# Performance work log

Hardware: AMD Instinct MI355X
Metric: run time of the kernel (lower is better)

The kernel has to match this reference:

```python
import jax, jax.numpy as jnp
import numpy as np

VOCAB, D_MODEL, HEADS, PAD_ID = 32000, 512, 8, 0
D_K = D_MODEL // HEADS
EPS = 1e-5


def pos_encoding(T, d):
    pos = jnp.arange(T, dtype=jnp.float32)[:, None]              # [T,1]
    freqs = 1.0 / (10000.0 ** (jnp.arange(0, d, 2, dtype=jnp.float32) / d))
    ang = pos * freqs                                            # [T,d/2]
    pe = jnp.zeros((T, d), dtype=jnp.float32)
    pe = pe.at[:, 0::2].set(jnp.sin(ang)).at[:, 1::2].set(jnp.cos(ang))
    return pe


def layer_norm(x, g, b):
    mu = jnp.mean(x, axis=-1, keepdims=True)
    var = jnp.var(x, axis=-1, keepdims=True)
    return (x - mu) * jax.lax.rsqrt(var + EPS) * g + b


def setup_inputs() -> dict:
    key = jax.random.key(0)
    ks = jax.random.split(key, 12)
    B, T = 4, 2048
    s = 0.02
    inp = {
        "tokens": jax.random.randint(ks[0], (B, T), 0, VOCAB),
        "emb": jax.random.normal(ks[1], (VOCAB, D_MODEL), jnp.float32) * s,
        "wq": jax.random.normal(ks[2], (D_MODEL, D_MODEL), jnp.float32) * s,
        "bq": jnp.zeros((D_MODEL,), jnp.float32),
        "wk": jax.random.normal(ks[3], (D_MODEL, D_MODEL), jnp.float32) * s,
        "bk": jnp.zeros((D_MODEL,), jnp.float32),
        "wv": jax.random.normal(ks[4], (D_MODEL, D_MODEL), jnp.float32) * s,
        "bv": jnp.zeros((D_MODEL,), jnp.float32),
        "wo": jax.random.normal(ks[5], (D_MODEL, D_MODEL), jnp.float32) * s,
        "bo": jnp.zeros((D_MODEL,), jnp.float32),
        "w1": jax.random.normal(ks[6], (D_MODEL, 2 * D_MODEL), jnp.float32) * s,
        "b1": jnp.zeros((2 * D_MODEL,), jnp.float32),
        "w2": jax.random.normal(ks[7], (2 * D_MODEL, D_MODEL), jnp.float32) * s,
        "b2": jnp.zeros((D_MODEL,), jnp.float32),
        "ln1_g": jnp.ones((D_MODEL,), jnp.float32),
        "ln1_b": jnp.zeros((D_MODEL,), jnp.float32),
        "ln2_g": jnp.ones((D_MODEL,), jnp.float32),
        "ln2_b": jnp.zeros((D_MODEL,), jnp.float32),
    }
    return inp


def reference(tokens, emb, wq, bq, wk, bk, wv, bv, wo, bo,
              w1, b1, w2, b2, ln1_g, ln1_b, ln2_g, ln2_b):
    B, T = tokens.shape
    x = emb[tokens] * jnp.sqrt(jnp.float32(D_MODEL))             # [B,T,D]
    x = x + pos_encoding(T, D_MODEL)[None]                       # add PE
    q = (x @ wq + bq).reshape(B, T, HEADS, D_K)
    k = (x @ wk + bk).reshape(B, T, HEADS, D_K)
    v = (x @ wv + bv).reshape(B, T, HEADS, D_K)
    scores = jnp.einsum("bqhd,bkhd->bhqk", q, k) / jnp.sqrt(jnp.float32(D_K))
    key_pad_mask = tokens == PAD_ID                              # [B,T]
    neg = jnp.finfo(scores.dtype).min
    scores = jnp.where(key_pad_mask[:, None, None, :], neg, scores)
    attn = jax.nn.softmax(scores, axis=-1)                       # [B,H,T,T]
    av = jnp.einsum("bhqk,bkhd->bqhd", attn, v).reshape(B, T, D_MODEL)
    av = av @ wo + bo
    h = layer_norm(av + x, ln1_g, ln1_b)
    ff = jax.nn.relu(h @ w1 + b1) @ w2 + b2
    out = layer_norm(h + ff, ln2_g, ln2_b)
    return out, key_pad_mask
```

## Files before the change

### kernel.cpp

```cpp
#include <hip/hip_runtime.h>
#include <hip/hip_bf16.h>
#include <math.h>

#define D_MODEL 512
#define HEADS   8
#define D_K     64
#define T_SEQ   2048
#define B_SZ    4
#define NROWS   (B_SZ * T_SEQ)
#define KVB     64

#define BM 128
#define BN 128
#define BKG 64

typedef __attribute__((ext_vector_type(8))) short short8;
typedef __attribute__((ext_vector_type(4))) float f32x4;
typedef __attribute__((ext_vector_type(4))) ushort bf16x4;
typedef __attribute__((ext_vector_type(4))) unsigned int u32x4;

typedef __attribute__((address_space(1))) const unsigned int as1_uint;
typedef __attribute__((address_space(3))) unsigned int as3_uint;

__device__ __forceinline__ ushort f2bf(float f) {
    union { float f; unsigned u; } v; v.f = f;
    unsigned u = v.u;
    unsigned r = (u + 0x7FFFu + ((u >> 16) & 1u)) >> 16;
    return (ushort)r;
}
__device__ __forceinline__ float bf2f(ushort u) {
    union { unsigned u; float f; } v; v.u = ((unsigned)u) << 16;
    return v.f;
}
__device__ __forceinline__ unsigned pk_bf16(float lo, float hi) {
    unsigned r;
    asm("v_cvt_pk_bf16_f32 %0, %1, %2" : "=v"(r) : "v"(lo), "v"(hi));
    return r;
}

__global__ __launch_bounds__(256) void k_prep(
    const int* __restrict__ tokens, const float* __restrict__ emb,
    const float* __restrict__ wq, const float* __restrict__ wk,
    const float* __restrict__ wv, const float* __restrict__ wo,
    const float* __restrict__ w1, const float* __restrict__ w2,
    const float* __restrict__ bq, const float* __restrict__ bk,
    const float* __restrict__ bv,
    ushort* __restrict__ xb, float* __restrict__ mask_out,
    ushort* __restrict__ wqkvT, ushort* __restrict__ woT,
    ushort* __restrict__ w1T, ushort* __restrict__ w2T,
    float* __restrict__ bqkv, float qsc)
{
    __shared__ ushort tls[32][33];
    int bid = blockIdx.x, tid = threadIdx.x;
    if (bid < 4096) {
        int row = bid * 2 + (tid >> 7);
        int t   = row & (T_SEQ - 1);
        int tok = tokens[row];
        int t2  = tid & 127;
        if (t2 == 0) mask_out[row] = (tok == 0) ? 1.0f : 0.0f;
        const float* e = emb + (size_t)tok * D_MODEL;
#pragma unroll
        for (int i = 0; i < 4; ++i) {
            int d = t2 + 128 * i;
            float freq = exp2f(-(float)(d & ~1) * 0.025952563240330564f);
            float sn, cs;
            sincosf((float)t * freq, &sn, &cs);
            float x = e[d] * 22.627416997969522f + ((d & 1) ? cs : sn);
            xb[(size_t)row * D_MODEL + d] = f2bf(x);
        }
        return;
    }
    const float* src; ushort* dst; float scale = 1.0f; int K, N, bx, by;
    if (bid < 5120) {
        int b = bid - 4096; int z = b >> 8; int rem = b & 255;
        bx = rem & 15; by = rem >> 4; K = 512; N = 512;
        src = (z == 0) ? wq : (z == 1) ? wk : (z == 2) ? wv : wo;
        dst = (z < 3) ? wqkvT + (size_t)z * 512 * 512 : woT;
        scale = (z == 0) ? qsc : 1.0f;
    } else if (bid < 5632) {
        int b = bid - 5120; bx = b & 31; by = b >> 5; K = 512; N = 1024; src = w1; dst = w1T;
    } else if (bid < 6144) {
        int b = bid - 5632; bx = b & 15; by = b >> 4; K = 1024; N = 512; src = w2; dst = w2T;
    } else {
        int i = (bid - 6144) * 256 + tid;
        if (i < 512)       bqkv[i] = bq[i] * qsc;
        else if (i < 1024) bqkv[i] = bk[i - 512];
        else if (i < 1536) bqkv[i] = bv[i - 1024];
        return;
    }
    int tx = tid & 31, ty = tid >> 5;
    int n0 = bx * 32, k0 = by * 32;
#pragma unroll
    for (int i = 0; i < 4; ++i)
        tls[ty + i * 8][tx] = f2bf(src[(size_t)(k0 + ty + i * 8) * N + n0 + tx] * scale);
    __syncthreads();
#pragma unroll
    for (int i = 0; i < 4; ++i)
        dst[(size_t)(n0 + ty + i * 8) * K + k0 + tx] = tls[tx][ty + i * 8];
}

template<int MODE, bool RELU>
__global__ __launch_bounds__(256) void k_gemm_lds(
    const ushort* __restrict__ A, const ushort* __restrict__ BT,
    const float* __restrict__ bias, void* __restrict__ C0,
    void* __restrict__ C1, void* __restrict__ C2,
    int M, int N, int K)
{
    __shared__ __attribute__((aligned(16))) ushort As[2][BM * BKG];
    __shared__ __attribute__((aligned(16))) ushort Bs[2][BN * BKG];

    const int tid = threadIdx.x;
    const int w = tid >> 6, l = tid & 63;
    const int lr = l & 15, lg = l >> 4;
    const int wr = w >> 1, wc = w & 1;

    int bx = blockIdx.x, by = blockIdx.y;
    {
        int nx = gridDim.x, ny = gridDim.y;
        if ((ny & 7) == 0) {
            int lin = bx + nx * by;
            int xcd = lin & 7, idx = lin >> 3;
            int per = ny >> 3;
            by = xcd * per + (idx % per);
            bx = idx / per;
        }
    }
    const int brow0 = by * BM;
    const int bcol0 = bx * BN;
    const int gi0 = w * 256 + l;
    const int swz = lr & 7;

    f32x4 acc[4][4] = {};
    const int nks = K >> 6;

#define STAGE(buf, k0)                                                          \
    {                                                                           \
        _Pragma("unroll")                                                       \
        for (int i = 0; i < 4; ++i) {                                           \
            int gi = gi0 + i * 64;                                              \
            int row = gi >> 3, slot = gi & 7;                                   \
            int g = slot ^ (row & 7);                                           \
            __builtin_amdgcn_global_load_lds(                                   \
                (as1_uint*)(A + (size_t)(brow0 + row) * K + (k0) + g * 8),      \
                (as3_uint*)(&As[buf][gi * 8]), 16, 0, 0);                       \
            __builtin_amdgcn_global_load_lds(                                   \
                (as1_uint*)(BT + (size_t)(bcol0 + row) * K + (k0) + g * 8),     \
                (as3_uint*)(&Bs[buf][gi * 8]), 16, 0, 0);                       \
        }                                                                       \
    }

    STAGE(0, 0);
    __syncthreads();

    int buf = 0;
    for (int ks = 0; ks < nks; ++ks) {
        if (ks + 1 < nks) STAGE(buf ^ 1, (ks + 1) * BKG);
#pragma unroll
        for (int kk = 0; kk < 2; ++kk) {
            short8 af[4], bfr[4];
#pragma unroll
            for (int m = 0; m < 4; ++m) {
                int row = wr * 64 + m * 16 + lr;
                int slot = (kk * 4 + lg) ^ swz;
                af[m] = *(const short8*)(&As[buf][row * 64 + slot * 8]);
            }
#pragma unroll
            for (int n = 0; n < 4; ++n) {
                int row = wc * 64 + n * 16 + lr;
                int slot = (kk * 4 + lg) ^ swz;
                bfr[n] = *(const short8*)(&Bs[buf][row * 64 + slot * 8]);
            }
#pragma unroll
            for (int m = 0; m < 4; ++m)
#pragma unroll
                for (int n = 0; n < 4; ++n)
                    acc[m][n] = __builtin_amdgcn_mfma_f32_16x16x32_bf16(af[m], bfr[n], acc[m][n], 0, 0, 0);
        }
        __syncthreads();
        buf ^= 1;
    }
#undef STAGE

#pragma unroll
    for (int n = 0; n < 4; ++n) {
        int col = bcol0 + wc * 64 + n * 16 + lr;
        float bv = bias[col];
#pragma unroll
        for (int m = 0; m < 4; ++m) {
            int row0 = brow0 + wr * 64 + m * 16 + 4 * lg;
            if constexpr (MODE == 2) {
                int seg = col >> 9, lc = col & 511;
                if (seg == 2) {
                    bf16x4 pk;
#pragma unroll
                    for (int j = 0; j < 4; ++j) pk[j] = f2bf(acc[m][n][j] + bv);
                    *(bf16x4*)((ushort*)C2 + (size_t)lc * M + row0) = pk;
                } else {
                    ushort* dst = (seg == 0) ? (ushort*)C0 : (ushort*)C1;
#pragma unroll
                    for (int j = 0; j < 4; ++j)
                        dst[(size_t)(row0 + j) * 512 + lc] = f2bf(acc[m][n][j] + bv);
                }
            } else if constexpr (MODE == 0) {
#pragma unroll
                for (int j = 0; j < 4; ++j) {
                    float v = acc[m][n][j] + bv;
                    if (RELU) v = fmaxf(v, 0.0f);
                    ((ushort*)C0)[(size_t)(row0 + j) * N + col] = f2bf(v);
                }
            } else {
#pragma unroll
                for (int j = 0; j < 4; ++j)
                    ((float*)C0)[(size_t)(row0 + j) * N + col] = acc[m][n][j] + bv;
            }
        }
    }
}

__global__ __launch_bounds__(512, 6) void k_attn(
    const ushort* __restrict__ Q, const ushort* __restrict__ Kb,
    const ushort* __restrict__ Vt, const int* __restrict__ tokens,
    ushort* __restrict__ Out)
{
    __shared__ __attribute__((aligned(16))) ushort Kl[2][KVB * 64];
    __shared__ __attribute__((aligned(16))) ushort Vl[2][KVB * 64];
    __shared__ __attribute__((aligned(16))) ushort Mbh[T_SEQ];
    __shared__ int padf[T_SEQ / KVB];

    const int tid = threadIdx.x;
    const int w = tid >> 6, l = tid & 63;
    const int lr = l & 15, lg = l >> 4;
    const int swz = lr & 7;

    int lin = blockIdx.x + 16 * (blockIdx.y + 8 * blockIdx.z);
    int xcd = lin & 7, idx = lin >> 3;
    int qt = idx & 15;
    int hb = xcd * 4 + (idx >> 4);
    int h = hb & 7, b = hb >> 3;

    const int q0 = qt * 128 + w * 16;

    const int gi   = w * 64 + l;
    const int srow = gi >> 3;
    const int sg   = gi & 7;
    const int sgx  = sg ^ (srow & 7);
    const ushort* Ksrc = Kb + ((size_t)(b * T_SEQ) + srow) * D_MODEL + h * D_K + sgx * 8;
    const int kbase = 32 * (sg >> 2) + 8 * ((sg >> 1) & 1) + 4 * (sg & 1);
    const ushort* Vsrc = Vt + (size_t)(h * D_K + srow) * NROWS + b * T_SEQ + kbase;
    const int vds = srow * 128 + sgx * 16;

#define KSTAGE(bufi, kt_)                                                       \
    __builtin_amdgcn_global_load_lds(                                           \
        (as1_uint*)(Ksrc + (size_t)(kt_) * KVB * D_MODEL),                      \
        (as3_uint*)(&Kl[bufi][gi * 8]), 16, 0, 0);

    const ushort* Qh = Q + (size_t)b * T_SEQ * D_MODEL + h * D_K;
    short8 aq[2];
#pragma unroll
    for (int c2 = 0; c2 < 2; ++c2)
        aq[c2] = *(const short8*)(Qh + (size_t)(q0 + lr) * D_MODEL + c2 * 32 + 8 * lg);

    const int* tk = tokens + b * T_SEQ;
#pragma unroll
    for (int it = 0; it < T_SEQ / 512; ++it) {
        int i = tid + it * 512;
        bool pad = (tk[i] == 0);
        Mbh[i] = pad ? (ushort)0xFF7F : (ushort)0;
        unsigned long long bal = __ballot(pad);
        if (l == 0) padf[it * 8 + w] = (bal != 0ull);
    }

    float l_run = 0.0f;
    f32x4 acc[4] = {};

    {
        bf16x4 va = *(const bf16x4*)(Vsrc);
        bf16x4 vb2 = *(const bf16x4*)(Vsrc + 16);
        KSTAGE(0, 0);
        u32x4 pk = { ((const unsigned*)&va)[0], ((const unsigned*)&va)[1],
                     ((const unsigned*)&vb2)[0], ((const unsigned*)&vb2)[1] };
        *(u32x4*)((char*)Vl[0] + vds) = pk;
    }
    __syncthreads();

    int buf = 0;
    const int NT = T_SEQ / KVB;
    for (int kt = 0; kt < NT; ++kt) {
        bf16x4 vna, vnb;
        bool more = (kt + 1 < NT);
        if (more) {
            KSTAGE(buf ^ 1, kt + 1);
            vna = *(const bf16x4*)(Vsrc + (kt + 1) * KVB);
            vnb = *(const bf16x4*)(Vsrc + (kt + 1) * KVB + 16);
        }

        const ushort* Kt = Kl[buf];
        const ushort* Vb = Vl[buf];

        f32x4 s[4];
        __builtin_amdgcn_s_setprio(1);
#pragma unroll
        for (int kb = 0; kb < 4; ++kb) {
            f32x4 sf = {};
#pragma unroll
            for (int c2 = 0; c2 < 2; ++c2) {
                short8 bk = *(const short8*)((const char*)Kt
                            + (kb * 16 + lr) * 128 + (((c2 * 4 + lg) ^ swz) * 16));
                sf = __builtin_amdgcn_mfma_f32_16x16x32_bf16(bk, aq[c2], sf, 0, 0, 0);
            }
            s[kb] = sf;
        }
        __builtin_amdgcn_s_setprio(0);

        if (padf[kt]) {
            const ushort* mrow = Mbh + kt * KVB + 4 * lg;
#pragma unroll
            for (int kb = 0; kb < 4; ++kb) {
                bf16x4 m4 = *(const bf16x4*)(mrow + kb * 16);
#pragma unroll
                for (int j = 0; j < 4; ++j) s[kb][j] += bf2f(m4[j]);
            }
        }

        float pv[4][4];
        float ts = 0.0f;
#pragma unroll
        for (int kb = 0; kb < 4; ++kb)
#pragma unroll
            for (int j = 0; j < 4; ++j) {
                float pe = exp2f(s[kb][j]);
                pv[kb][j] = pe;
                ts += pe;
            }
        ts += __shfl_xor(ts, 16);
        ts += __shfl_xor(ts, 32);
        l_run += ts;

        unsigned dw[4][2];
#pragma unroll
        for (int kb = 0; kb < 4; ++kb) {
            dw[kb][0] = pk_bf16(pv[kb][0], pv[kb][1]);
            dw[kb][1] = pk_bf16(pv[kb][2], pv[kb][3]);
        }
        u32x4 pw0 = { dw[0][0], dw[0][1], dw[1][0], dw[1][1] };
        u32x4 pw1 = { dw[2][0], dw[2][1], dw[3][0], dw[3][1] };
        short8 pa0 = __builtin_bit_cast(short8, pw0);
        short8 pa1 = __builtin_bit_cast(short8, pw1);

        __builtin_amdgcn_s_setprio(1);
#pragma unroll
        for (int c = 0; c < 4; ++c) {
            short8 bv0 = *(const short8*)((const char*)Vb
                         + (c * 16 + lr) * 128 + ((lg ^ swz) * 16));
            acc[c] = __builtin_amdgcn_mfma_f32_16x16x32_bf16(bv0, pa0, acc[c], 0, 0, 0);
            short8 bv1 = *(const short8*)((const char*)Vb
                         + (c * 16 + lr) * 128 + (((4 + lg) ^ swz) * 16));
            acc[c] = __builtin_amdgcn_mfma_f32_16x16x32_bf16(bv1, pa1, acc[c], 0, 0, 0);
        }
        __builtin_amdgcn_s_setprio(0);

        if (more) {
            u32x4 pk = { ((const unsigned*)&vna)[0], ((const unsigned*)&vna)[1],
                         ((const unsigned*)&vnb)[0], ((const unsigned*)&vnb)[1] };
            *(u32x4*)((char*)Vl[buf ^ 1] + vds) = pk;
        }
        __syncthreads();
        buf ^= 1;
    }
#undef KSTAGE

    float rl = 1.0f / l_run;
    ushort* orow = Out + (size_t)(b * T_SEQ + q0 + lr) * D_MODEL + h * D_K;
#pragma unroll
    for (int c = 0; c < 4; ++c) {
        bf16x4 pk;
#pragma unroll
        for (int j = 0; j < 4; ++j) pk[j] = f2bf(acc[c][j] * rl);
        *(bf16x4*)(orow + c * 16 + 4 * lg) = pk;
    }
}

template<bool A_BF16, bool RES_BF16, bool OUT_F32>
__global__ __launch_bounds__(256) void k_ln(
    const void* __restrict__ A, const void* __restrict__ Res,
    const float* __restrict__ g, const float* __restrict__ bb,
    float* __restrict__ of, ushort* __restrict__ ob)
{
    int row = blockIdx.x * 4 + (threadIdx.x >> 6);
    int l = threadIdx.x & 63;
    float v[8];
    float s = 0.0f, ss = 0.0f;
#pragma unroll
    for (int i = 0; i < 2; ++i) {
        int d0 = i * 256 + l * 4;
        f32x4 va, vb;
        if (A_BF16) {
            bf16x4 t = *(const bf16x4*)((const ushort*)A + (size_t)row * D_MODEL + d0);
#pragma unroll
            for (int j = 0; j < 4; ++j) va[j] = bf2f(t[j]);
        } else {
            va = *(const f32x4*)((const float*)A + (size_t)row * D_MODEL + d0);
        }
        if (RES_BF16) {
            bf16x4 t = *(const bf16x4*)((const ushort*)Res + (size_t)row * D_MODEL + d0);
#pragma unroll
            for (int j = 0; j < 4; ++j) vb[j] = bf2f(t[j]);
        } else {
            vb = *(const f32x4*)((const float*)Res + (size_t)row * D_MODEL + d0);
        }
#pragma unroll
        for (int j = 0; j < 4; ++j) {
            float x = va[j] + vb[j];
            v[i * 4 + j] = x; s += x; ss += x * x;
        }
    }
#pragma unroll
    for (int d = 1; d < 64; d <<= 1) { s += __shfl_xor(s, d); ss += __shfl_xor(ss, d); }
    float mu  = s * (1.0f / 512.0f);
    float var = ss * (1.0f / 512.0f) - mu * mu;
    float rs  = rsqrtf(var + 1e-5f);
#pragma unroll
    for (int i = 0; i < 2; ++i)
#pragma unroll
        for (int j = 0; j < 4; ++j) {
            int d = i * 256 + l * 4 + j;
            float o = (v[i * 4 + j] - mu) * rs * g[d] + bb[d];
            if (OUT_F32) of[(size_t)row * D_MODEL + d] = o;
            else         ob[(size_t)row * D_MODEL + d] = f2bf(o);
        }
}

extern "C" void kernel_launch(void* const* d_in, const int* in_sizes, int n_in,
                              void* d_out, int out_size, void* d_ws, size_t ws_size,
                              hipStream_t stream)
{
    const int*   tokens = (const int*)  d_in[0];
    const float* emb    = (const float*)d_in[1];
    const float* wq     = (const float*)d_in[2];
    const float* bq     = (const float*)d_in[3];
    const float* wk     = (const float*)d_in[4];
    const float* bk     = (const float*)d_in[5];
    const float* wv     = (const float*)d_in[6];
    const float* bv     = (const float*)d_in[7];
    const float* wo     = (const float*)d_in[8];
    const float* bo     = (const float*)d_in[9];
    const float* w1     = (const float*)d_in[10];
    const float* b1     = (const float*)d_in[11];
    const float* w2     = (const float*)d_in[12];
    const float* b2     = (const float*)d_in[13];
    const float* ln1_g  = (const float*)d_in[14];
    const float* ln1_b  = (const float*)d_in[15];
    const float* ln2_g  = (const float*)d_in[16];
    const float* ln2_b  = (const float*)d_in[17];

    char* ws = (char*)d_ws;
    ushort* xb   = (ushort*)(ws + 0);
    ushort* Qb   = (ushort*)(ws + 8388608);
    ushort* Kbuf = (ushort*)(ws + 16777216);
    ushort* Vt   = (ushort*)(ws + 25165824);
    ushort* atb  = (ushort*)(ws + 33554432);
    ushort* AVb  = (ushort*)(ws + 41943040);
    ushort* wqkvT = (ushort*)(ws + 50331648);
    ushort* woT  = wqkvT + 1536 * 512;
    ushort* w1T  = woT + 262144;
    ushort* w2T  = w1T + 524288;
    float*  bqkv = (float*)(w2T + 524288);

    ushort* hb   = Qb;
    ushort* ff1b = Kbuf;
    ushort* ff2b = AVb;

    float* out_f    = (float*)d_out;
    float* mask_out = out_f + (size_t)NROWS * D_MODEL;

    const float QSC = 0.18033688011112042f;

    k_prep<<<6150, 256, 0, stream>>>(
        tokens, emb, wq, wk, wv, wo, w1, w2, bq, bk, bv,
        xb, mask_out, wqkvT, woT, w1T, w2T, bqkv, QSC);

    k_gemm_lds<2, false><<<dim3(12, 64), 256, 0, stream>>>(
        xb, wqkvT, bqkv, Qb, Kbuf, Vt, NROWS, 1536, 512);

    k_attn<<<dim3(T_SEQ / 128, HEADS, B_SZ), 512, 0, stream>>>(Qb, Kbuf, Vt, tokens, atb);

    k_gemm_lds<0, false><<<dim3(4, 64), 256, 0, stream>>>(
        atb, woT, bo, AVb, nullptr, nullptr, NROWS, 512, 512);

    k_ln<true, true, false><<<NROWS / 4, 256, 0, stream>>>(
        AVb, xb, ln1_g, ln1_b, nullptr, hb);

    k_gemm_lds<0, true><<<dim3(8, 64), 256, 0, stream>>>(
        hb, w1T, b1, ff1b, nullptr, nullptr, NROWS, 1024, 512);
    k_gemm_lds<0, false><<<dim3(4, 64), 256, 0, stream>>>(
        ff1b, w2T, b2, ff2b, nullptr, nullptr, NROWS, 512, 1024);

    k_ln<true, true, true><<<NROWS / 4, 256, 0, stream>>>(
        ff2b, hb, ln2_g, ln2_b, out_f, nullptr);
}
```

Measured before the change: 159.4 us.

## Split attention key range in two and merge partial outputs in a combine kernel

The attention kernel now splits the key sequence into two halves, which doubles the number of thread blocks, and raises the occupancy hint in the launch bounds. Each block writes an unnormalized bf16 partial output and its row-sum to workspace. A new combine kernel adds the two partials and divides by the summed normalizers. The aim is better CU occupancy and load balance across the GPU. In exchange it adds a second launch, extra global traffic for the partials, and extra bf16 rounding on the unnormalized values.

After: 165.8 us. 4.0% more time.

```diff
diff --git a/kernel.cpp b/kernel.cpp
--- a/kernel.cpp
+++ b/kernel.cpp
@@ -9,6 +9,8 @@
 #define B_SZ    4
 #define NROWS   (B_SZ * T_SEQ)
 #define KVB     64
+#define KSPLIT  2
+#define KHALF   (T_SEQ / KSPLIT)
 
 #define BM 128
 #define BN 128
@@ -217,36 +219,40 @@
     }
 }
 
-__global__ __launch_bounds__(512, 6) void k_attn(
+__global__ __launch_bounds__(512, 8) void k_attn(
     const ushort* __restrict__ Q, const ushort* __restrict__ Kb,
     const ushort* __restrict__ Vt, const int* __restrict__ tokens,
-    ushort* __restrict__ Out)
+    ushort* __restrict__ O0, ushort* __restrict__ O1,
+    float* __restrict__ lp)
 {
     __shared__ __attribute__((aligned(16))) ushort Kl[2][KVB * 64];
     __shared__ __attribute__((aligned(16))) ushort Vl[2][KVB * 64];
-    __shared__ __attribute__((aligned(16))) ushort Mbh[T_SEQ];
-    __shared__ int padf[T_SEQ / KVB];
+    __shared__ __attribute__((aligned(16))) ushort Mbh[KHALF];
+    __shared__ int padf[KHALF / KVB];
 
     const int tid = threadIdx.x;
     const int w = tid >> 6, l = tid & 63;
     const int lr = l & 15, lg = l >> 4;
     const int swz = lr & 7;
 
-    int lin = blockIdx.x + 16 * (blockIdx.y + 8 * blockIdx.z);
+    int lin = blockIdx.x + 16 * blockIdx.y + 256 * blockIdx.z;
     int xcd = lin & 7, idx = lin >> 3;
+    int group = xcd + 8 * (idx >> 4);
     int qt = idx & 15;
-    int hb = xcd * 4 + (idx >> 4);
-    int h = hb & 7, b = hb >> 3;
-
-    const int q0 = qt * 128 + w * 16;
+    int ks = group & 1;
+    int h  = (group >> 1) & 7;
+    int b  = group >> 4;
+
+    const int q0  = qt * 128 + w * 16;
+    const int kb0 = ks * KHALF;
 
     const int gi   = w * 64 + l;
     const int srow = gi >> 3;
     const int sg   = gi & 7;
     const int sgx  = sg ^ (srow & 7);
-    const ushort* Ksrc = Kb + ((size_t)(b * T_SEQ) + srow) * D_MODEL + h * D_K + sgx * 8;
+    const ushort* Ksrc = Kb + ((size_t)(b * T_SEQ + kb0) + srow) * D_MODEL + h * D_K + sgx * 8;
     const int kbase = 32 * (sg >> 2) + 8 * ((sg >> 1) & 1) + 4 * (sg & 1);
-    const ushort* Vsrc = Vt + (size_t)(h * D_K + srow) * NROWS + b * T_SEQ + kbase;
+    const ushort* Vsrc = Vt + (size_t)(h * D_K + srow) * NROWS + b * T_SEQ + kb0 + kbase;
     const int vds = srow * 128 + sgx * 16;
 
 #define KSTAGE(bufi, kt_)                                                       \
@@ -260,9 +266,9 @@
     for (int c2 = 0; c2 < 2; ++c2)
         aq[c2] = *(const short8*)(Qh + (size_t)(q0 + lr) * D_MODEL + c2 * 32 + 8 * lg);
 
-    const int* tk = tokens + b * T_SEQ;
-#pragma unroll
-    for (int it = 0; it < T_SEQ / 512; ++it) {
+    const int* tk = tokens + b * T_SEQ + kb0;
+#pragma unroll
+    for (int it = 0; it < KHALF / 512; ++it) {
         int i = tid + it * 512;
         bool pad = (tk[i] == 0);
         Mbh[i] = pad ? (ushort)0xFF7F : (ushort)0;
@@ -284,7 +290,7 @@
     __syncthreads();
 
     int buf = 0;
-    const int NT = T_SEQ / KVB;
+    const int NT = KHALF / KVB;
     for (int kt = 0; kt < NT; ++kt) {
         bf16x4 vna, vnb;
         bool more = (kt + 1 < NT);
@@ -369,15 +375,37 @@
     }
 #undef KSTAGE
 
-    float rl = 1.0f / l_run;
-    ushort* orow = Out + (size_t)(b * T_SEQ + q0 + lr) * D_MODEL + h * D_K;
+    ushort* Op = (ks == 0) ? O0 : O1;
+    ushort* orow = Op + (size_t)(b * T_SEQ + q0 + lr) * D_MODEL + h * D_K;
 #pragma unroll
     for (int c = 0; c < 4; ++c) {
         bf16x4 pk;
 #pragma unroll
-        for (int j = 0; j < 4; ++j) pk[j] = f2bf(acc[c][j] * rl);
+        for (int j = 0; j < 4; ++j) pk[j] = f2bf(acc[c][j]);
         *(bf16x4*)(orow + c * 16 + 4 * lg) = pk;
     }
+    if (l < 16)
+        lp[(size_t)(ks * 8 + h) * NROWS + b * T_SEQ + q0 + l] = l_run;
+}
+
+__global__ __launch_bounds__(256) void k_comb(
+    ushort* __restrict__ O0, const ushort* __restrict__ O1,
+    const float* __restrict__ lp)
+{
+    int g = blockIdx.x * 256 + threadIdx.x;
+    int row = g >> 6, seg = g & 63;
+    int h = seg >> 3;
+    size_t off = (size_t)row * D_MODEL + seg * 8;
+    short8 a = *(const short8*)(O0 + off);
+    short8 c = *(const short8*)(O1 + off);
+    float l0 = lp[(size_t)h * NROWS + row];
+    float l1 = lp[(size_t)(8 + h) * NROWS + row];
+    float rl = 1.0f / (l0 + l1);
+    short8 r;
+#pragma unroll
+    for (int i = 0; i < 8; ++i)
+        r[i] = (short)f2bf((bf2f((ushort)a[i]) + bf2f((ushort)c[i])) * rl);
+    *(short8*)(O0 + off) = r;
 }
 
 template<bool A_BF16, bool RES_BF16, bool OUT_F32>
@@ -465,6 +493,7 @@
     ushort* w1T  = woT + 262144;
     ushort* w2T  = w1T + 524288;
     float*  bqkv = (float*)(w2T + 524288);
+    float*  lpart = bqkv + 2048;
 
     ushort* hb   = Qb;
     ushort* ff1b = Kbuf;
@@ -482,7 +511,9 @@
     k_gemm_lds<2, false><<<dim3(12, 64), 256, 0, stream>>>(
         xb, wqkvT, bqkv, Qb, Kbuf, Vt, NROWS, 1536, 512);
 
-    k_attn<<<dim3(T_SEQ / 128, HEADS, B_SZ), 512, 0, stream>>>(Qb, Kbuf, Vt, tokens, atb);
+    k_attn<<<dim3(16, 16, 4), 512, 0, stream>>>(
+        Qb, Kbuf, Vt, tokens, atb, AVb, lpart);
+    k_comb<<<2048, 256, 0, stream>>>(atb, AVb, lpart);
 
     k_gemm_lds<0, false><<<dim3(4, 64), 256, 0, stream>>>(
         atb, woT, bo, AVb, nullptr, nullptr, NROWS, 512, 512);
```
